# Optimization experiments

Measured on AMD Instinct MI355X. Metric: run time of the kernel, lower is better.

## Reference

```python
import jax, jax.numpy as jnp
import numpy as np

H = 256
L = 5
N = 50000


def setup_inputs() -> dict:
    key = jax.random.key(0)
    ks = jax.random.split(key, 12)
    E = 800000
    x = jax.random.normal(ks[0], (N, H), dtype=jnp.float32)
    edge_index = jax.random.randint(ks[1], (2, E), 0, N, dtype=jnp.int64)
    edge_weight = jax.random.uniform(ks[2], (E,), dtype=jnp.float32)
    s = 1.0 / np.sqrt(H)
    weight = jax.random.uniform(ks[3], (L, H, H), dtype=jnp.float32, minval=-s, maxval=s)
    w_ih = jax.random.uniform(ks[4], (3 * H, H), dtype=jnp.float32, minval=-s, maxval=s)
    w_hh = jax.random.uniform(ks[5], (3 * H, H), dtype=jnp.float32, minval=-s, maxval=s)
    b_ih = jax.random.uniform(ks[6], (3 * H,), dtype=jnp.float32, minval=-s, maxval=s)
    b_hh = jax.random.uniform(ks[7], (3 * H,), dtype=jnp.float32, minval=-s, maxval=s)
    fc_w = jax.random.uniform(ks[8], (1, H), dtype=jnp.float32, minval=-s, maxval=s)
    fc_b = jax.random.uniform(ks[9], (1,), dtype=jnp.float32, minval=-s, maxval=s)
    return {"x": x, "edge_index": edge_index, "edge_weight": edge_weight,
            "weight": weight, "w_ih": w_ih, "w_hh": w_hh, "b_ih": b_ih,
            "b_hh": b_hh, "fc_w": fc_w, "fc_b": fc_b, "prob": 0}


def _gru_cell(m, h, w_ih, w_hh, b_ih, b_hh):
    # PyTorch GRUCell: gates ordered (r, z, n)
    gi = m @ w_ih.T + b_ih  # [N, 3H]
    gh = h @ w_hh.T + b_hh  # [N, 3H]
    r = jax.nn.sigmoid(gi[:, :H] + gh[:, :H])
    z = jax.nn.sigmoid(gi[:, H:2 * H] + gh[:, H:2 * H])
    n = jnp.tanh(gi[:, 2 * H:] + r * gh[:, 2 * H:])
    return (1.0 - z) * n + z * h


def reference(x, edge_index, edge_weight, weight, w_ih, w_hh, b_ih, b_hh, fc_w, fc_b, prob):
    src = edge_index[0]
    dst = edge_index[1]
    h = x
    for i in range(L):
        m = h @ weight[i]                       # [N, H] per-layer linear transform
        msg = edge_weight[:, None] * m[src]     # [E, H] gather + edge weighting
        agg = jax.ops.segment_sum(msg, dst, num_segments=N)  # scatter-add
        h = _gru_cell(agg, h, w_ih, w_hh, b_ih, b_hh)
    h = jax.nn.relu(h)
    # dropout with p=prob; reference runs deterministically with p=0 (eval mode)
    out = h @ fc_w.T + fc_b                     # [N, 1]
    return out
```

## Files before the change

kernel.cpp:

```cpp
#include <hip/hip_runtime.h>
#include <hip/hip_bf16.h>
#include <math.h>


#define HDIM 256

using bf16x8 = __attribute__((ext_vector_type(8))) short;
using f32x4  = __attribute__((ext_vector_type(4))) float;

__device__ __forceinline__ bf16x8 ldfrag(const ushort* p) {
    union { uint4 u; bf16x8 f; } x;
    x.u = *(const uint4*)p;
    return x.f;
}
#define MFMA(a, b, c) __builtin_amdgcn_mfma_f32_16x16x32_bf16((a), (b), (c), 0, 0, 0)
#define GLD16(g, l)                                                            \
    __builtin_amdgcn_global_load_lds(                                          \
        (const __attribute__((address_space(1))) void*)(g),                    \
        (__attribute__((address_space(3))) void*)(l), 16, 0, 0)

__device__ __forceinline__ float ldf(const void* p, size_t i, int isbf) {
    if (isbf) return __bfloat162float(((const __hip_bfloat16*)p)[i]);
    return ((const float*)p)[i];
}
__device__ __forceinline__ ushort f2bs(float v) {
    __hip_bfloat16 b = __float2bfloat16(v);
    return *(ushort*)&b;
}
__device__ __forceinline__ float bs2f(ushort u) {
    __hip_bfloat16 b = *(__hip_bfloat16*)&u;
    return __bfloat162float(b);
}
__device__ __forceinline__ size_t taddrH(int n, int k) {
    return (size_t)(n >> 4) * 4096 + (size_t)((k >> 5) << 9)
         + (size_t)(((k >> 3) & 3) << 7) + (size_t)((n & 15) << 3) + (k & 7);
}
__device__ __forceinline__ size_t taddrA(int n, int k) {
    return (size_t)(n >> 4) * 8192 + (size_t)((k >> 5) << 9)
         + (size_t)(((k >> 3) & 3) << 7) + (size_t)((n & 15) << 3) + (k & 7);
}

__global__ void detect_k(const void* x, const void* ei, int* flags) {
    if (blockIdx.x == 0 && threadIdx.x == 0) {
        const __hip_bfloat16* xb = (const __hip_bfloat16*)x;
        int isbf = 1;
        for (int i = 0; i < 1024; ++i) {
            float v = fabsf(__bfloat162float(xb[i]));
            if (!(v < 1e6f)) { isbf = 0; break; }
        }
        flags[0] = isbf;
        const int* e32 = (const int*)ei;
        int orv = e32[1] | e32[3] | e32[5] | e32[7] | e32[9] | e32[11];
        flags[1] = (orv == 0) ? 1 : 0;
    }
}

__global__ void conv_h0_k(const void* x, ushort* HH, ushort* HL,
                          const int* flags, int useHL, int Nn, size_t npad256) {
    size_t i = (size_t)blockIdx.x * blockDim.x + threadIdx.x;
    if (i >= npad256) return;
    const int n = (int)(i >> 8), k = (int)(i & 255);
    float v = 0.f;
    if (n < Nn) v = ldf(x, i, flags[0]);
    const ushort hi = f2bs(v);
    const size_t a = taddrH(n, k);
    HH[a] = hi;
    if (useHL) HL[a] = f2bs(v - bs2f(hi));
}

__global__ void prep_k(const void* w, const void* wih, const void* whh,
                       const void* bih, const void* bhh,
                       ushort* BgH, ushort* BgL, ushort* BwH, ushort* BwL,
                       float* bsum, float* bni, float* bnh,
                       const int* flags, int L) {
    int i = blockIdx.x * blockDim.x + threadIdx.x;
    int isbf = flags[0];
    if (i < 1048576) {
        const int j = i >> 10, k = i & 1023;
        const int g = (j >> 4) & 3, b = ((j >> 6) << 4) + (j & 15);
        const int kk = k & 255, seg = k >> 8;
        float v = 0.f;
        if (g == 0) v = (seg < 2) ? ldf(wih, (size_t)b * 256 + kk, isbf)
                                  : ldf(whh, (size_t)b * 256 + kk, isbf);
        else if (g == 1) v = (seg < 2) ? ldf(wih, (size_t)(256 + b) * 256 + kk, isbf)
                                       : ldf(whh, (size_t)(256 + b) * 256 + kk, isbf);
        else if (g == 2) v = (seg < 2) ? ldf(wih, (size_t)(512 + b) * 256 + kk, isbf) : 0.f;
        else             v = (seg < 2) ? 0.f : ldf(whh, (size_t)(512 + b) * 256 + kk, isbf);
        const ushort hi = f2bs(v);
        const int ct = j >> 4, c = k >> 5;
        const size_t a = (size_t)(ct * 32 + c) * 512
                       + (size_t)(((k >> 3) & 3) << 7) + ((j & 15) << 3) + (k & 7);
        BgH[a] = hi; BgL[a] = f2bs(v - bs2f(hi));
    }
    if (i < L * 131072) {
        const int l = i >> 17, r2 = i & 131071;
        const int j = r2 >> 9, k = r2 & 511;
        const int kk = k & 255;
        const float v = ldf(w, ((size_t)l << 16) + (size_t)kk * 256 + j, isbf);
        const ushort hi = f2bs(v);
        const int ct = j >> 4, c = k >> 5;
        const size_t a = (size_t)l * 131072 + (size_t)(ct * 16 + c) * 512
                       + (size_t)(((k >> 3) & 3) << 7) + ((j & 15) << 3) + (k & 7);
        BwH[a] = hi; BwL[a] = f2bs(v - bs2f(hi));
    }
    if (i < 512) bsum[i] = ldf(bih, i, isbf) + ldf(bhh, i, isbf);
    if (i < 256) {
        bni[i] = ldf(bih, 512 + i, isbf);
        bnh[i] = ldf(bhh, 512 + i, isbf);
    }
}


__global__ void zero_int_k(int* p, int n) {
    int i = blockIdx.x * blockDim.x + threadIdx.x;
    if (i < n) p[i] = 0;
}

__global__ void count_k(const void* ei, int* cnt, const int* flags, int E) {
    int e = blockIdx.x * blockDim.x + threadIdx.x;
    if (e >= E) return;
    const int* e32 = (const int*)ei;
    int d = flags[1] ? e32[2 * ((size_t)E + e)] : e32[(size_t)E + e];
    atomicAdd(&cnt[d], 1);
}

__global__ __launch_bounds__(256)
void scan1_k(const int* cnt, int* ptr, int* bsumN, int N) {
    __shared__ int s[256];
    const int t = threadIdx.x;
    const int gid = blockIdx.x * 256 + t;
    int v = (gid < N) ? cnt[gid] : 0;
    const int own = v;
    s[t] = v;
    __syncthreads();
#pragma unroll
    for (int off = 1; off < 256; off <<= 1) {
        int add = (t >= off) ? s[t - off] : 0;
        __syncthreads();
        s[t] += add;
        __syncthreads();
    }
    if (gid < N) ptr[gid] = s[t] - own;
    if (t == 255) bsumN[blockIdx.x] = s[255];
}

__global__ __launch_bounds__(256)
void scan2_k(int* bsumN, int NB) {
    __shared__ int s[256];
    __shared__ int carry;
    const int t = threadIdx.x;
    if (t == 0) carry = 0;
    __syncthreads();
    for (int base = 0; base < NB; base += 256) {
        const int i = base + t;
        int v = (i < NB) ? bsumN[i] : 0;
        const int own = v;
        s[t] = v;
        __syncthreads();
#pragma unroll
        for (int off = 1; off < 256; off <<= 1) {
            int add = (t >= off) ? s[t - off] : 0;
            __syncthreads();
            s[t] += add;
            __syncthreads();
        }
        if (i < NB) bsumN[i] = carry + s[t] - own;
        __syncthreads();
        if (t == 0) carry += s[255];
        __syncthreads();
    }
}

__global__ void scan3_k(int* ptr, int* cursor, const int* bsumN, int N, int E) {
    const int gid = blockIdx.x * 256 + threadIdx.x;
    if (gid < N) {
        const int p = ptr[gid] + bsumN[blockIdx.x];
        ptr[gid] = p;
        cursor[gid] = p;
    }
    if (gid == 0) ptr[N] = E;
}

__global__ void fill_k(const void* ei, const void* ew, int* cursor,
                       int* srcs, float* wse, const int* flags, int E) {
    int e = blockIdx.x * blockDim.x + threadIdx.x;
    if (e >= E) return;
    const int* e32 = (const int*)ei;
    int s, d;
    if (flags[1]) { s = e32[2 * (size_t)e]; d = e32[2 * ((size_t)E + e)]; }
    else          { s = e32[e];             d = e32[(size_t)E + e]; }
    const int p = atomicAdd(&cursor[d], 1);
    srcs[p] = s;
    wse[p] = ldf(ew, e, flags[0]);
}

__global__ __launch_bounds__(256)
void spmm_k(const float* __restrict__ m, const int* __restrict__ ptr,
            const int* __restrict__ srcs, const float* __restrict__ wse,
            ushort* __restrict__ AGG, int N) {
    const int node = blockIdx.x * 4 + (threadIdx.x >> 6);
    if (node >= N) return;
    const int lane4 = (threadIdx.x & 63) << 2;
    const int p0 = ptr[node], p1 = ptr[node + 1];
    float4 acc = make_float4(0.f, 0.f, 0.f, 0.f);
    int j = p0;
    for (; j + 1 < p1; j += 2) {
        const int s0 = srcs[j], s1 = srcs[j + 1];
        const float w0 = wse[j], w1 = wse[j + 1];
        const float4 v0 = *(const float4*)&m[(size_t)s0 * HDIM + lane4];
        const float4 v1 = *(const float4*)&m[(size_t)s1 * HDIM + lane4];
        acc.x = fmaf(w0, v0.x, acc.x); acc.y = fmaf(w0, v0.y, acc.y);
        acc.z = fmaf(w0, v0.z, acc.z); acc.w = fmaf(w0, v0.w, acc.w);
        acc.x = fmaf(w1, v1.x, acc.x); acc.y = fmaf(w1, v1.y, acc.y);
        acc.z = fmaf(w1, v1.z, acc.z); acc.w = fmaf(w1, v1.w, acc.w);
    }
    if (j < p1) {
        const int s0 = srcs[j];
        const float w0 = wse[j];
        const float4 v0 = *(const float4*)&m[(size_t)s0 * HDIM + lane4];
        acc.x = fmaf(w0, v0.x, acc.x); acc.y = fmaf(w0, v0.y, acc.y);
        acc.z = fmaf(w0, v0.z, acc.z); acc.w = fmaf(w0, v0.w, acc.w);
    }
    ushort4 hi, lo;
    hi.x = f2bs(acc.x); lo.x = f2bs(acc.x - bs2f(hi.x));
    hi.y = f2bs(acc.y); lo.y = f2bs(acc.y - bs2f(hi.y));
    hi.z = f2bs(acc.z); lo.z = f2bs(acc.z - bs2f(hi.z));
    hi.w = f2bs(acc.w); lo.w = f2bs(acc.w - bs2f(hi.w));
    *(ushort4*)&AGG[taddrA(node, lane4)] = hi;
    *(ushort4*)&AGG[taddrA(node, 256 + lane4)] = lo;
}

__global__ __launch_bounds__(256)
void m_gemm_k(const ushort* __restrict__ HH, const ushort* __restrict__ HL,
              const ushort* __restrict__ BwHl, const ushort* __restrict__ BwLl,
              float* __restrict__ m, const int* __restrict__ flags,
              int useHL, int nRB) {
    __shared__ ushort lds[12288];
    const int rb = blockIdx.x >> 1, cgB = blockIdx.x & 1;
    if (rb >= nRB) return;
    const int tid = threadIdx.x, lane = tid & 63;
    const int wv = __builtin_amdgcn_readfirstlane(tid >> 6);
    const int wr = wv & 1, wc = wv >> 1;
    const int lm = lane & 15, lq = lane >> 4;
    const int fullsplit = !flags[0];
    const int NCH = useHL ? 16 : 8;
    const int rt = rb * 8, t0 = 2 * wv;
    f32x4 acc[4][4];
#pragma unroll
    for (int i = 0; i < 4; ++i)
#pragma unroll
        for (int j = 0; j < 4; ++j) acc[i][j] = (f32x4){0.f, 0.f, 0.f, 0.f};

    for (int c = 0; c < NCH; ++c) {
        __syncthreads();
        const ushort* a0 = (c < 8)
            ? HH + (size_t)(rt + t0) * 4096 + (size_t)c * 512
            : HL + (size_t)(rt + t0) * 4096 + (size_t)(c - 8) * 512;
        GLD16(a0 + (size_t)lane * 8, &lds[t0 * 512]);
        GLD16(a0 + 4096 + (size_t)lane * 8, &lds[t0 * 512 + 512]);
        const size_t bb = ((size_t)(8 * cgB + t0) * 16 + c) * 512;
        GLD16(BwHl + bb + (size_t)lane * 8, &lds[4096 + t0 * 512]);
        GLD16(BwHl + bb + 8192 + (size_t)lane * 8, &lds[4096 + t0 * 512 + 512]);
        if (fullsplit) {
            GLD16(BwLl + bb + (size_t)lane * 8, &lds[8192 + t0 * 512]);
            GLD16(BwLl + bb + 8192 + (size_t)lane * 8, &lds[8192 + t0 * 512 + 512]);
        }
        __syncthreads();
        bf16x8 af[4], bf[4];
#pragma unroll
        for (int i = 0; i < 4; ++i)
            af[i] = ldfrag(&lds[(4 * wr + i) * 512 + lq * 128 + lm * 8]);
#pragma unroll
        for (int j = 0; j < 4; ++j)
            bf[j] = ldfrag(&lds[4096 + (4 * wc + j) * 512 + lq * 128 + lm * 8]);
#pragma unroll
        for (int i = 0; i < 4; ++i)
#pragma unroll
            for (int j = 0; j < 4; ++j) acc[i][j] = MFMA(af[i], bf[j], acc[i][j]);
        if (fullsplit) {
#pragma unroll
            for (int j = 0; j < 4; ++j) {
                const bf16x8 bl = ldfrag(&lds[8192 + (4 * wc + j) * 512 + lq * 128 + lm * 8]);
#pragma unroll
                for (int i = 0; i < 4; ++i) acc[i][j] = MFMA(af[i], bl, acc[i][j]);
            }
        }
    }
#pragma unroll
    for (int i = 0; i < 4; ++i) {
        const int row = rb * 128 + wr * 64 + i * 16 + lq * 4;
#pragma unroll
        for (int j = 0; j < 4; ++j) {
            const int col = cgB * 128 + wc * 64 + j * 16 + lm;
#pragma unroll
            for (int v = 0; v < 4; ++v)
                m[(size_t)(row + v) * 256 + col] = acc[i][j][v];
        }
    }
}

__global__ __launch_bounds__(256)
void gates_k(const ushort* __restrict__ AGG,
             const ushort* __restrict__ HH, const ushort* __restrict__ HL,
             const ushort* __restrict__ BgH, const ushort* __restrict__ BgL,
             const float* __restrict__ bsum, const float* __restrict__ bni,
             const float* __restrict__ bnh,
             ushort* __restrict__ HnH, ushort* __restrict__ HnL,
             const int* __restrict__ flags, int useHL, int nRB) {
    __shared__ ushort lds[12288];
    const int x = blockIdx.x & 7, rem = blockIdx.x >> 3;
    const int cgB = rem & 7, rbHi = rem >> 3;
    const int rb = rbHi * 8 + x;
    if (rb >= nRB) return;
    const int tid = threadIdx.x, lane = tid & 63;
    const int wv = __builtin_amdgcn_readfirstlane(tid >> 6);
    const int wr = wv & 1, wc = wv >> 1;
    const int lm = lane & 15, lq = lane >> 4;
    const int fullsplit = !flags[0];
    const int NCH = useHL ? 32 : 24;
    const int rt = rb * 8, t0 = 2 * wv;
    f32x4 acc[4][4];
#pragma unroll
    for (int i = 0; i < 4; ++i)
#pragma unroll
        for (int j = 0; j < 4; ++j) acc[i][j] = (f32x4){0.f, 0.f, 0.f, 0.f};

    for (int c = 0; c < NCH; ++c) {
        __syncthreads();
        const ushort* a0;
        size_t stride;
        if (c < 16)      { a0 = AGG + (size_t)(rt + t0) * 8192 + (size_t)c * 512; stride = 8192; }
        else if (c < 24) { a0 = HH + (size_t)(rt + t0) * 4096 + (size_t)(c - 16) * 512; stride = 4096; }
        else             { a0 = HL + (size_t)(rt + t0) * 4096 + (size_t)(c - 24) * 512; stride = 4096; }
        GLD16(a0 + (size_t)lane * 8, &lds[t0 * 512]);
        GLD16(a0 + stride + (size_t)lane * 8, &lds[t0 * 512 + 512]);
        const size_t bb = ((size_t)(8 * cgB + t0) * 32 + c) * 512;
        GLD16(BgH + bb + (size_t)lane * 8, &lds[4096 + t0 * 512]);
        GLD16(BgH + bb + 16384 + (size_t)lane * 8, &lds[4096 + t0 * 512 + 512]);
        if (fullsplit) {
            GLD16(BgL + bb + (size_t)lane * 8, &lds[8192 + t0 * 512]);
            GLD16(BgL + bb + 16384 + (size_t)lane * 8, &lds[8192 + t0 * 512 + 512]);
        }
        __syncthreads();
        bf16x8 af[4], bf[4];
#pragma unroll
        for (int i = 0; i < 4; ++i)
            af[i] = ldfrag(&lds[(4 * wr + i) * 512 + lq * 128 + lm * 8]);
#pragma unroll
        for (int j = 0; j < 4; ++j)
            bf[j] = ldfrag(&lds[4096 + (4 * wc + j) * 512 + lq * 128 + lm * 8]);
#pragma unroll
        for (int i = 0; i < 4; ++i)
#pragma unroll
            for (int j = 0; j < 4; ++j) acc[i][j] = MFMA(af[i], bf[j], acc[i][j]);
        if (fullsplit) {
#pragma unroll
            for (int j = 0; j < 4; ++j) {
                const bf16x8 bl = ldfrag(&lds[8192 + (4 * wc + j) * 512 + lq * 128 + lm * 8]);
#pragma unroll
                for (int i = 0; i < 4; ++i) acc[i][j] = MFMA(af[i], bl, acc[i][j]);
            }
        }
    }
    const int b = (2 * cgB + wc) * 16 + lm;
    const float rbias = bsum[b], zbias = bsum[256 + b];
    const float ibias = bni[b], hbias = bnh[b];
#pragma unroll
    for (int i = 0; i < 4; ++i) {
        const int row0 = rb * 128 + wr * 64 + i * 16 + lq * 4;
#pragma unroll
        for (int v = 0; v < 4; ++v) {
            const int row = row0 + v;
            const size_t ho = taddrH(row, b);
            float hold = bs2f(HH[ho]);
            if (useHL) hold += bs2f(HL[ho]);
            const float r = 1.f / (1.f + expf(-(acc[i][0][v] + rbias)));
            const float z = 1.f / (1.f + expf(-(acc[i][1][v] + zbias)));
            const float nn = tanhf(acc[i][2][v] + ibias + r * (acc[i][3][v] + hbias));
            const float hv = (1.f - z) * nn + z * hold;
            const ushort hi = f2bs(hv);
            HnH[ho] = hi;
            if (useHL) HnL[ho] = f2bs(hv - bs2f(hi));
        }
    }
}

__global__ void final_k(const ushort* __restrict__ HH, const ushort* __restrict__ HL,
                        const void* fcw, const void* fcb,
                        void* out, const int* flags, int useHL, int N) {
    const int n = blockIdx.x;
    const int t = threadIdx.x;
    const int isbf = flags[0];
    const size_t off = taddrH(n, t);
    float h = bs2f(HH[off]);
    if (useHL) h += bs2f(HL[off]);
    float v = fmaxf(h, 0.f) * ldf(fcw, t, isbf);
#pragma unroll
    for (int offx = 32; offx >= 1; offx >>= 1) v += __shfl_down(v, offx);
    __shared__ float red[4];
    if ((t & 63) == 0) red[t >> 6] = v;
    __syncthreads();
    if (t == 0) {
        const float s = red[0] + red[1] + red[2] + red[3] + ldf(fcb, 0, isbf);
        if (isbf) ((__hip_bfloat16*)out)[n] = __float2bfloat16(s);
        else      ((float*)out)[n] = s;
    }
}

extern "C" void kernel_launch(void* const* d_in, const int* in_sizes, int n_in,
                              void* d_out, int out_size, void* d_ws, size_t ws_size,
                              hipStream_t stream) {
    const int H = HDIM;
    const int N = in_sizes[0] / H;
    const int E = in_sizes[2];
    const int L = in_sizes[3] / (H * H);
    const int NB = (N + 255) / 256;
    const int nRB = (N + 127) / 128;
    const size_t NPAD = (size_t)nRB * 128;
    const size_t hHalf = NPAD * 256;
    const size_t aggHalf = NPAD * 512;

    char* p = (char*)d_ws;
    int*    flags = (int*)p;              p += 64;
    ushort* AGG  = (ushort*)p;            p += aggHalf * 2;
    ushort* HxH  = (ushort*)p;            p += hHalf * 2;
    ushort* HyH  = (ushort*)p;            p += hHalf * 2;
    float*  m    = (float*)p;             p += NPAD * 256 * 4;
    ushort* BgH  = (ushort*)p;            p += (size_t)1048576 * 2;
    ushort* BgL  = (ushort*)p;            p += (size_t)1048576 * 2;
    ushort* BwH  = (ushort*)p;            p += (size_t)L * 131072 * 2;
    ushort* BwL  = (ushort*)p;            p += (size_t)L * 131072 * 2;
    float*  bsum = (float*)p;             p += 512 * 4;
    float*  bni  = (float*)p;             p += 256 * 4;
    float*  bnh  = (float*)p;             p += 256 * 4;
    int*    ptr  = (int*)p;               p += (size_t)(N + 1) * 4;
    int*    cursor = (int*)p;             p += (size_t)N * 4;
    int*    bsumN  = (int*)p;             p += (size_t)NB * 4;
    int*    srcs   = (int*)p;             p += (size_t)E * 4;
    float*  wse    = (float*)p;           p += (size_t)E * 4;
    const size_t need_reduced = (size_t)(p - (char*)d_ws);
    ushort* HxL = (ushort*)p;
    ushort* HyL = (ushort*)(p + hHalf * 2);
    const size_t need_full = need_reduced + 2 * hHalf * 2;
    const int useHL = (ws_size >= need_full) ? 1 : 0;
    if (!useHL) { HxL = HxH; HyL = HyH; }

    detect_k<<<dim3(1), dim3(64), 0, stream>>>(d_in[0], d_in[1], flags);
    conv_h0_k<<<dim3((unsigned)NPAD), dim3(256), 0, stream>>>(
        d_in[0], HxH, HxL, flags, useHL, N, NPAD * 256);
    prep_k<<<dim3(4096), dim3(256), 0, stream>>>(
        d_in[3], d_in[4], d_in[5], d_in[6], d_in[7],
        BgH, BgL, BwH, BwL, bsum, bni, bnh, flags, L);

    zero_int_k<<<dim3(NB), dim3(256), 0, stream>>>(cursor, N);
    count_k<<<dim3((E + 255) / 256), dim3(256), 0, stream>>>(d_in[1], cursor, flags, E);
    scan1_k<<<dim3(NB), dim3(256), 0, stream>>>(cursor, ptr, bsumN, N);
    scan2_k<<<dim3(1), dim3(256), 0, stream>>>(bsumN, NB);
    scan3_k<<<dim3(NB), dim3(256), 0, stream>>>(ptr, cursor, bsumN, N, E);
    fill_k<<<dim3((E + 255) / 256), dim3(256), 0, stream>>>(
        d_in[1], d_in[2], cursor, srcs, wse, flags, E);

    const dim3 blk(256);
    const unsigned gGrid = 64u * (unsigned)((nRB + 7) / 8);
    ushort *HcH = HxH, *HcL = HxL, *HnH = HyH, *HnL = HyL;
    for (int l = 0; l < L; ++l) {
        m_gemm_k<<<dim3((unsigned)(2 * nRB)), blk, 0, stream>>>(
            HcH, HcL, BwH + (size_t)l * 131072, BwL + (size_t)l * 131072,
            m, flags, useHL, nRB);
        spmm_k<<<dim3((N + 3) / 4), blk, 0, stream>>>(m, ptr, srcs, wse, AGG, N);
        gates_k<<<dim3(gGrid), blk, 0, stream>>>(
            AGG, HcH, HcL, BgH, BgL, bsum, bni, bnh, HnH, HnL, flags, useHL, nRB);
        ushort* t;
        t = HcH; HcH = HnH; HnH = t;
        t = HcL; HcL = HnL; HnL = t;
    }
    final_k<<<dim3(N), blk, 0, stream>>>(
        HcH, HcL, d_in[8], d_in[9], d_out, flags, useHL, N);
}
```

Baseline: 2.299 ms.

## Double K-chunk per barrier in GEMMs, unroll SpMM by 4, fast gate activations

```diff
diff --git a/kernel.cpp b/kernel.cpp
--- a/kernel.cpp
+++ b/kernel.cpp
@@ -30,6 +30,12 @@
 __device__ __forceinline__ float bs2f(ushort u) {
     __hip_bfloat16 b = *(__hip_bfloat16*)&u;
     return __bfloat162float(b);
+}
+__device__ __forceinline__ float sigm(float x) {
+    return __builtin_amdgcn_rcpf(1.f + __expf(-x));
+}
+__device__ __forceinline__ float ftanh(float x) {
+    return 2.f * __builtin_amdgcn_rcpf(1.f + __expf(-2.f * x)) - 1.f;
 }
 __device__ __forceinline__ size_t taddrH(int n, int k) {
     return (size_t)(n >> 4) * 4096 + (size_t)((k >> 5) << 9)
@@ -204,17 +210,23 @@
     const int p0 = ptr[node], p1 = ptr[node + 1];
     float4 acc = make_float4(0.f, 0.f, 0.f, 0.f);
     int j = p0;
-    for (; j + 1 < p1; j += 2) {
-        const int s0 = srcs[j], s1 = srcs[j + 1];
-        const float w0 = wse[j], w1 = wse[j + 1];
+    for (; j + 3 < p1; j += 4) {
+        const int s0 = srcs[j], s1 = srcs[j + 1], s2 = srcs[j + 2], s3 = srcs[j + 3];
+        const float w0 = wse[j], w1 = wse[j + 1], w2 = wse[j + 2], w3 = wse[j + 3];
         const float4 v0 = *(const float4*)&m[(size_t)s0 * HDIM + lane4];
         const float4 v1 = *(const float4*)&m[(size_t)s1 * HDIM + lane4];
+        const float4 v2 = *(const float4*)&m[(size_t)s2 * HDIM + lane4];
+        const float4 v3 = *(const float4*)&m[(size_t)s3 * HDIM + lane4];
         acc.x = fmaf(w0, v0.x, acc.x); acc.y = fmaf(w0, v0.y, acc.y);
         acc.z = fmaf(w0, v0.z, acc.z); acc.w = fmaf(w0, v0.w, acc.w);
         acc.x = fmaf(w1, v1.x, acc.x); acc.y = fmaf(w1, v1.y, acc.y);
         acc.z = fmaf(w1, v1.z, acc.z); acc.w = fmaf(w1, v1.w, acc.w);
-    }
-    if (j < p1) {
+        acc.x = fmaf(w2, v2.x, acc.x); acc.y = fmaf(w2, v2.y, acc.y);
+        acc.z = fmaf(w2, v2.z, acc.z); acc.w = fmaf(w2, v2.w, acc.w);
+        acc.x = fmaf(w3, v3.x, acc.x); acc.y = fmaf(w3, v3.y, acc.y);
+        acc.z = fmaf(w3, v3.z, acc.z); acc.w = fmaf(w3, v3.w, acc.w);
+    }
+    for (; j < p1; ++j) {
         const int s0 = srcs[j];
         const float w0 = wse[j];
         const float4 v0 = *(const float4*)&m[(size_t)s0 * HDIM + lane4];
@@ -235,7 +247,7 @@
               const ushort* __restrict__ BwHl, const ushort* __restrict__ BwLl,
               float* __restrict__ m, const int* __restrict__ flags,
               int useHL, int nRB) {
-    __shared__ ushort lds[12288];
+    __shared__ ushort lds[16384];
     const int rb = blockIdx.x >> 1, cgB = blockIdx.x & 1;
     if (rb >= nRB) return;
     const int tid = threadIdx.x, lane = tid & 63;
@@ -243,7 +255,7 @@
     const int wr = wv & 1, wc = wv >> 1;
     const int lm = lane & 15, lq = lane >> 4;
     const int fullsplit = !flags[0];
-    const int NCH = useHL ? 16 : 8;
+    const int NIT = useHL ? 8 : 4;
     const int rt = rb * 8, t0 = 2 * wv;
     f32x4 acc[4][4];
 #pragma unroll
@@ -251,38 +263,43 @@
 #pragma unroll
         for (int j = 0; j < 4; ++j) acc[i][j] = (f32x4){0.f, 0.f, 0.f, 0.f};
 
-    for (int c = 0; c < NCH; ++c) {
-        __syncthreads();
-        const ushort* a0 = (c < 8)
-            ? HH + (size_t)(rt + t0) * 4096 + (size_t)c * 512
-            : HL + (size_t)(rt + t0) * 4096 + (size_t)(c - 8) * 512;
-        GLD16(a0 + (size_t)lane * 8, &lds[t0 * 512]);
-        GLD16(a0 + 4096 + (size_t)lane * 8, &lds[t0 * 512 + 512]);
-        const size_t bb = ((size_t)(8 * cgB + t0) * 16 + c) * 512;
-        GLD16(BwHl + bb + (size_t)lane * 8, &lds[4096 + t0 * 512]);
-        GLD16(BwHl + bb + 8192 + (size_t)lane * 8, &lds[4096 + t0 * 512 + 512]);
-        if (fullsplit) {
-            GLD16(BwLl + bb + (size_t)lane * 8, &lds[8192 + t0 * 512]);
-            GLD16(BwLl + bb + 8192 + (size_t)lane * 8, &lds[8192 + t0 * 512 + 512]);
-        }
-        __syncthreads();
-        bf16x8 af[4], bf[4];
-#pragma unroll
-        for (int i = 0; i < 4; ++i)
-            af[i] = ldfrag(&lds[(4 * wr + i) * 512 + lq * 128 + lm * 8]);
-#pragma unroll
-        for (int j = 0; j < 4; ++j)
-            bf[j] = ldfrag(&lds[4096 + (4 * wc + j) * 512 + lq * 128 + lm * 8]);
-#pragma unroll
-        for (int i = 0; i < 4; ++i)
-#pragma unroll
-            for (int j = 0; j < 4; ++j) acc[i][j] = MFMA(af[i], bf[j], acc[i][j]);
-        if (fullsplit) {
-#pragma unroll
-            for (int j = 0; j < 4; ++j) {
-                const bf16x8 bl = ldfrag(&lds[8192 + (4 * wc + j) * 512 + lq * 128 + lm * 8]);
-#pragma unroll
-                for (int i = 0; i < 4; ++i) acc[i][j] = MFMA(af[i], bl, acc[i][j]);
+    for (int t = 0; t < NIT; ++t) {
+        __syncthreads();
+        const ushort* ab = (t < 4) ? HH : HL;
+        const int cA = (t < 4) ? 2 * t : 2 * (t - 4);
+        const size_t a0 = (size_t)(rt + t0) * 4096 + (size_t)cA * 512 + (size_t)lane * 8;
+        GLD16(ab + a0, &lds[(t0 * 2 + 0) * 512]);
+        GLD16(ab + a0 + 512, &lds[(t0 * 2 + 1) * 512]);
+        GLD16(ab + a0 + 4096, &lds[((t0 + 1) * 2 + 0) * 512]);
+        GLD16(ab + a0 + 4608, &lds[((t0 + 1) * 2 + 1) * 512]);
+        const size_t bb0 = ((size_t)(8 * cgB + t0) * 16 + 2 * t) * 512 + (size_t)lane * 8;
+        GLD16(BwHl + bb0, &lds[8192 + (t0 * 2 + 0) * 512]);
+        GLD16(BwHl + bb0 + 512, &lds[8192 + (t0 * 2 + 1) * 512]);
+        GLD16(BwHl + bb0 + 8192, &lds[8192 + ((t0 + 1) * 2 + 0) * 512]);
+        GLD16(BwHl + bb0 + 8704, &lds[8192 + ((t0 + 1) * 2 + 1) * 512]);
+        __syncthreads();
+#pragma unroll
+        for (int cc = 0; cc < 2; ++cc) {
+            bf16x8 af[4], bf[4];
+#pragma unroll
+            for (int i = 0; i < 4; ++i)
+                af[i] = ldfrag(&lds[((4 * wr + i) * 2 + cc) * 512 + lq * 128 + lm * 8]);
+#pragma unroll
+            for (int j = 0; j < 4; ++j)
+                bf[j] = ldfrag(&lds[8192 + ((4 * wc + j) * 2 + cc) * 512 + lq * 128 + lm * 8]);
+#pragma unroll
+            for (int i = 0; i < 4; ++i)
+#pragma unroll
+                for (int j = 0; j < 4; ++j) acc[i][j] = MFMA(af[i], bf[j], acc[i][j]);
+            if (fullsplit) {
+#pragma unroll
+                for (int j = 0; j < 4; ++j) {
+                    const bf16x8 bl = ldfrag(
+                        &BwLl[((size_t)(8 * cgB + 4 * wc + j) * 16 + 2 * t + cc) * 512
+                              + lq * 128 + lm * 8]);
+#pragma unroll
+                    for (int i = 0; i < 4; ++i) acc[i][j] = MFMA(af[i], bl, acc[i][j]);
+                }
             }
         }
     }
@@ -307,7 +324,7 @@
              const float* __restrict__ bnh,
              ushort* __restrict__ HnH, ushort* __restrict__ HnL,
              const int* __restrict__ flags, int useHL, int nRB) {
-    __shared__ ushort lds[12288];
+    __shared__ ushort lds[16384];
     const int x = blockIdx.x & 7, rem = blockIdx.x >> 3;
     const int cgB = rem & 7, rbHi = rem >> 3;
     const int rb = rbHi * 8 + x;
@@ -317,7 +334,7 @@
     const int wr = wv & 1, wc = wv >> 1;
     const int lm = lane & 15, lq = lane >> 4;
     const int fullsplit = !flags[0];
-    const int NCH = useHL ? 32 : 24;
+    const int NIT = useHL ? 16 : 12;
     const int rt = rb * 8, t0 = 2 * wv;
     f32x4 acc[4][4];
 #pragma unroll
@@ -325,40 +342,47 @@
 #pragma unroll
         for (int j = 0; j < 4; ++j) acc[i][j] = (f32x4){0.f, 0.f, 0.f, 0.f};
 
-    for (int c = 0; c < NCH; ++c) {
-        __syncthreads();
-        const ushort* a0;
+    for (int t = 0; t < NIT; ++t) {
+        __syncthreads();
+        const ushort* ab;
         size_t stride;
-        if (c < 16)      { a0 = AGG + (size_t)(rt + t0) * 8192 + (size_t)c * 512; stride = 8192; }
-        else if (c < 24) { a0 = HH + (size_t)(rt + t0) * 4096 + (size_t)(c - 16) * 512; stride = 4096; }
-        else             { a0 = HL + (size_t)(rt + t0) * 4096 + (size_t)(c - 24) * 512; stride = 4096; }
-        GLD16(a0 + (size_t)lane * 8, &lds[t0 * 512]);
-        GLD16(a0 + stride + (size_t)lane * 8, &lds[t0 * 512 + 512]);
-        const size_t bb = ((size_t)(8 * cgB + t0) * 32 + c) * 512;
-        GLD16(BgH + bb + (size_t)lane * 8, &lds[4096 + t0 * 512]);
-        GLD16(BgH + bb + 16384 + (size_t)lane * 8, &lds[4096 + t0 * 512 + 512]);
-        if (fullsplit) {
-            GLD16(BgL + bb + (size_t)lane * 8, &lds[8192 + t0 * 512]);
-            GLD16(BgL + bb + 16384 + (size_t)lane * 8, &lds[8192 + t0 * 512 + 512]);
-        }
-        __syncthreads();
-        bf16x8 af[4], bf[4];
-#pragma unroll
-        for (int i = 0; i < 4; ++i)
-            af[i] = ldfrag(&lds[(4 * wr + i) * 512 + lq * 128 + lm * 8]);
-#pragma unroll
-        for (int j = 0; j < 4; ++j)
-            bf[j] = ldfrag(&lds[4096 + (4 * wc + j) * 512 + lq * 128 + lm * 8]);
-#pragma unroll
-        for (int i = 0; i < 4; ++i)
-#pragma unroll
-            for (int j = 0; j < 4; ++j) acc[i][j] = MFMA(af[i], bf[j], acc[i][j]);
-        if (fullsplit) {
-#pragma unroll
-            for (int j = 0; j < 4; ++j) {
-                const bf16x8 bl = ldfrag(&lds[8192 + (4 * wc + j) * 512 + lq * 128 + lm * 8]);
-#pragma unroll
-                for (int i = 0; i < 4; ++i) acc[i][j] = MFMA(af[i], bl, acc[i][j]);
+        int cA;
+        if (t < 8)       { ab = AGG; stride = 8192; cA = 2 * t; }
+        else if (t < 12) { ab = HH;  stride = 4096; cA = 2 * (t - 8); }
+        else             { ab = HL;  stride = 4096; cA = 2 * (t - 12); }
+        const size_t a0 = (size_t)(rt + t0) * stride + (size_t)cA * 512 + (size_t)lane * 8;
+        GLD16(ab + a0, &lds[(t0 * 2 + 0) * 512]);
+        GLD16(ab + a0 + 512, &lds[(t0 * 2 + 1) * 512]);
+        GLD16(ab + a0 + stride, &lds[((t0 + 1) * 2 + 0) * 512]);
+        GLD16(ab + a0 + stride + 512, &lds[((t0 + 1) * 2 + 1) * 512]);
+        const size_t bb0 = ((size_t)(8 * cgB + t0) * 32 + 2 * t) * 512 + (size_t)lane * 8;
+        GLD16(BgH + bb0, &lds[8192 + (t0 * 2 + 0) * 512]);
+        GLD16(BgH + bb0 + 512, &lds[8192 + (t0 * 2 + 1) * 512]);
+        GLD16(BgH + bb0 + 16384, &lds[8192 + ((t0 + 1) * 2 + 0) * 512]);
+        GLD16(BgH + bb0 + 16896, &lds[8192 + ((t0 + 1) * 2 + 1) * 512]);
+        __syncthreads();
+#pragma unroll
+        for (int cc = 0; cc < 2; ++cc) {
+            bf16x8 af[4], bf[4];
+#pragma unroll
+            for (int i = 0; i < 4; ++i)
+                af[i] = ldfrag(&lds[((4 * wr + i) * 2 + cc) * 512 + lq * 128 + lm * 8]);
+#pragma unroll
+            for (int j = 0; j < 4; ++j)
+                bf[j] = ldfrag(&lds[8192 + ((4 * wc + j) * 2 + cc) * 512 + lq * 128 + lm * 8]);
+#pragma unroll
+            for (int i = 0; i < 4; ++i)
+#pragma unroll
+                for (int j = 0; j < 4; ++j) acc[i][j] = MFMA(af[i], bf[j], acc[i][j]);
+            if (fullsplit) {
+#pragma unroll
+                for (int j = 0; j < 4; ++j) {
+                    const bf16x8 bl = ldfrag(
+                        &BgL[((size_t)(8 * cgB + 4 * wc + j) * 32 + 2 * t + cc) * 512
+                             + lq * 128 + lm * 8]);
+#pragma unroll
+                    for (int i = 0; i < 4; ++i) acc[i][j] = MFMA(af[i], bl, acc[i][j]);
+                }
             }
         }
     }
@@ -374,9 +398,9 @@
             const size_t ho = taddrH(row, b);
             float hold = bs2f(HH[ho]);
             if (useHL) hold += bs2f(HL[ho]);
-            const float r = 1.f / (1.f + expf(-(acc[i][0][v] + rbias)));
-            const float z = 1.f / (1.f + expf(-(acc[i][1][v] + zbias)));
-            const float nn = tanhf(acc[i][2][v] + ibias + r * (acc[i][3][v] + hbias));
+            const float r = sigm(acc[i][0][v] + rbias);
+            const float z = sigm(acc[i][1][v] + zbias);
+            const float nn = ftanh(acc[i][2][v] + ibias + r * (acc[i][3][v] + hbias));
             const float hv = (1.f - z) * nn + z * hold;
             const ushort hi = f2bs(hv);
             HnH[ho] = hi;
```

Measured after the change: 2.508 ms. 1.09x slower.
